# Performance work log

Measured on AMD Instinct MI355X. Metric: run time of the kernel, lower is better.

The kernel has to match this reference:

```python
import jax, jax.numpy as jnp
import numpy as np

NUM_EXPERTS = 8
TOP_K = 2
DIM = 1024
HIDDEN = 2048
TOKENS = 8192


def setup_inputs() -> dict:
    key = jax.random.key(0)
    k0, k1, k2, k3, k4 = jax.random.split(key, 5)
    x = jax.random.normal(k0, (TOKENS, DIM), dtype=jnp.float32)
    gate_w = jax.random.normal(k1, (NUM_EXPERTS, DIM), dtype=jnp.float32) * 0.02
    # SwiGLU expert weights, stacked over experts
    w1 = jax.random.normal(k2, (NUM_EXPERTS, DIM, HIDDEN), dtype=jnp.float32) * 0.02
    w3 = jax.random.normal(k3, (NUM_EXPERTS, DIM, HIDDEN), dtype=jnp.float32) * 0.02
    w2 = jax.random.normal(k4, (NUM_EXPERTS, HIDDEN, DIM), dtype=jnp.float32) * 0.02
    return {"x": x, "gate_w": gate_w, "w1": w1, "w3": w3, "w2": w2}


def reference(x, gate_w, w1, w3, w2):
    # x: [T, D]; gate_w: [E, D]; w1,w3: [E, D, H]; w2: [E, H, D]
    E = gate_w.shape[0]
    gate_logits = x @ gate_w.T                               # [T, E]
    topk_vals, topk_idx = jax.lax.top_k(gate_logits, TOP_K)  # [T, K]
    topk_w = jax.nn.softmax(topk_vals.astype(jnp.float32), axis=-1).astype(x.dtype)
    # per-token per-expert combine weight: sum_k w[t,k] * [sel[t,k]==e]  -> [T, E]
    combine = jnp.einsum('tk,tke->te', topk_w,
                         jax.nn.one_hot(topk_idx, E, dtype=x.dtype))
    # SwiGLU experts, computed per expert over all tokens then masked-combined
    h = jnp.einsum('td,edh->eth', x, w1)                     # [E, T, H]
    g = jnp.einsum('td,edh->eth', x, w3)                     # [E, T, H]
    y = jnp.einsum('eth,ehd->etd', jax.nn.silu(h) * g, w2)   # [E, T, D]
    return jnp.einsum('te,etd->td', combine, y)              # [T, D]
```

## Files before the change

### kernel.cpp

```cpp
#include <hip/hip_runtime.h>
#include <cstdint>
#include <cstddef>

#define T_TOKENS 8192
#define DIM      1024
#define HID      2048
#define NE       8
#define HCAP     17408

typedef __attribute__((ext_vector_type(8))) short short8;
typedef __attribute__((ext_vector_type(4))) short short4v;
typedef __attribute__((ext_vector_type(4))) float f32x4;

__device__ __forceinline__ unsigned short f2bf(float f) {
  unsigned int u = __builtin_bit_cast(unsigned int, f);
  u += 0x7fffu + ((u >> 16) & 1u);
  return (unsigned short)(u >> 16);
}

__device__ __forceinline__ void gload16(const void* g, void* lds) {
  __builtin_amdgcn_global_load_lds((const __attribute__((address_space(1))) void*)g,
                                   (__attribute__((address_space(3))) void*)lds,
                                   16, 0, 0);
}

#define PREP_GATE0 12288
__device__ __forceinline__ void transcvt_body(
    const float* __restrict__ in, unsigned short* __restrict__ out,
    int K, int N, int bx, int by, int e, float (*tile)[65], int tid) {
  int r  = tid >> 2;
  int c0 = (tid & 3) * 16;
  const float* src = in + ((size_t)e * K + by * 64 + r) * N + bx * 64 + c0;
#pragma unroll
  for (int j = 0; j < 4; j++) {
    float4 v = *(const float4*)(src + j * 4);
    tile[r][c0 + j * 4 + 0] = v.x; tile[r][c0 + j * 4 + 1] = v.y;
    tile[r][c0 + j * 4 + 2] = v.z; tile[r][c0 + j * 4 + 3] = v.w;
  }
  __syncthreads();
  short8 o0, o1;
#pragma unroll
  for (int j = 0; j < 8; j++) o0[j] = (short)f2bf(tile[c0 + j][r]);
#pragma unroll
  for (int j = 0; j < 8; j++) o1[j] = (short)f2bf(tile[c0 + 8 + j][r]);
  unsigned short* dst = out + ((size_t)e * N + bx * 64 + r) * K + by * 64 + c0;
  *(short8*)dst = o0;
  *(short8*)(dst + 8) = o1;
}

__global__ __launch_bounds__(256) void prep_kernel(
    const float* __restrict__ x, const float* __restrict__ gw,
    const float* __restrict__ w1, const float* __restrict__ w3,
    const float* __restrict__ w2,
    unsigned short* __restrict__ W1T, unsigned short* __restrict__ W3T,
    unsigned short* __restrict__ W2T,
    int2* __restrict__ sel, float2* __restrict__ wts,
    unsigned short* __restrict__ xb) {
  __shared__ float tile[64][65];
  int bid = blockIdx.x, tid = threadIdx.x;

  if (bid < PREP_GATE0) {
    if (bid < 4096) {
      int t = bid;
      transcvt_body(w1, W1T, DIM, HID, t % 32, (t / 32) % 16, t / 512, tile, tid);
    } else if (bid < 8192) {
      int t = bid - 4096;
      transcvt_body(w3, W3T, DIM, HID, t % 32, (t / 32) % 16, t / 512, tile, tid);
    } else {
      int t = bid - 8192;
      transcvt_body(w2, W2T, HID, DIM, t % 16, (t / 16) % 32, t / 512, tile, tid);
    }
    return;
  }

  int wid = tid >> 6, lane = tid & 63;
  int t = (bid - PREP_GATE0) * 4 + wid;
  const float* xr = x + (size_t)t * DIM;
  unsigned short* xo = xb + (size_t)t * DIM;
  double acc[NE];
#pragma unroll
  for (int e = 0; e < NE; e++) acc[e] = 0.0;
#pragma unroll
  for (int p = 0; p < 4; p++) {
    int idx = p * 256 + lane * 4;
    float4 xv = *(const float4*)(xr + idx);
    short4v o;
    o[0] = (short)f2bf(xv.x); o[1] = (short)f2bf(xv.y);
    o[2] = (short)f2bf(xv.z); o[3] = (short)f2bf(xv.w);
    *(short4v*)(xo + idx) = o;
#pragma unroll
    for (int e = 0; e < NE; e++) {
      float4 g = *(const float4*)(gw + e * DIM + idx);
      acc[e] += (double)xv.x * (double)g.x + (double)xv.y * (double)g.y
              + (double)xv.z * (double)g.z + (double)xv.w * (double)g.w;
    }
  }
#pragma unroll
  for (int e = 0; e < NE; e++) {
    double v = acc[e];
#pragma unroll
    for (int off = 32; off > 0; off >>= 1) v += __shfl_xor(v, off);
    acc[e] = v;
  }
  if (lane == 0) {
    float l[NE];
#pragma unroll
    for (int e = 0; e < NE; e++) l[e] = (float)acc[e];
    int i0 = 0; float v0 = l[0];
#pragma unroll
    for (int e = 1; e < NE; e++) if (l[e] > v0) { v0 = l[e]; i0 = e; }
    int i1 = -1; float v1 = -3.4e38f;
#pragma unroll
    for (int e = 0; e < NE; e++) if (e != i0 && l[e] > v1) { v1 = l[e]; i1 = e; }
    float ew = __expf(v1 - v0);
    float w0 = 1.0f / (1.0f + ew);
    float w1v = ew / (1.0f + ew);
    sel[t] = make_int2(i0, i1);
    wts[t] = make_float2(w0, w1v);
  }
}

__global__ void scatter_kernel(const int2* __restrict__ sel, const float2* __restrict__ wts,
                               int* __restrict__ cnt, int* __restrict__ btok,
                               float* __restrict__ bw) {
  __shared__ int hist[NE];
  __shared__ int base[NE];
  int tid = threadIdx.x;
  if (tid < NE) hist[tid] = 0;
  __syncthreads();
  int t = blockIdx.x * 256 + tid;
  int2 s = sel[t]; float2 w = wts[t];
  int p0 = atomicAdd(&hist[s.x], 1);
  int p1 = atomicAdd(&hist[s.y], 1);
  __syncthreads();
  if (tid < NE) base[tid] = atomicAdd(&cnt[tid], hist[tid]);
  __syncthreads();
  int o0 = base[s.x] + p0;
  btok[s.x * T_TOKENS + o0] = t; bw[s.x * T_TOKENS + o0] = w.x;
  int o1 = base[s.y] + p1;
  btok[s.y * T_TOKENS + o1] = t; bw[s.y * T_TOKENS + o1] = w.y;
}

__global__ __launch_bounds__(256, 2) void gemm1_kernel(
    const unsigned short* __restrict__ xb, const unsigned short* __restrict__ w1t,
    const unsigned short* __restrict__ w3t, const int* __restrict__ cnt,
    const int* __restrict__ btok, const unsigned short* __restrict__ zbuf,
    unsigned short* __restrict__ h) {
  int e = blockIdx.z;
  int cn = cnt[e];
  int pc = (cn + 127) & ~127;
  int mt = blockIdx.y;
  if (mt * 128 >= pc) return;
  int hoff = 0;
#pragma unroll
  for (int i = 0; i < NE; i++) { int pi = (cnt[i] + 127) & ~127; if (i < e) hoff += pi; }
  int nt = blockIdx.x;

  __shared__ short8 At8[1024];
  __shared__ short8 B18[512];
  __shared__ short8 B38[512];

  int tid = threadIdx.x, wid = tid >> 6, lane = tid & 63;
  int m0 = mt * 128;

  int swzcol = ((lane & 7) ^ (lane >> 3)) * 8;

  const unsigned short* asrc[4];
#pragma unroll
  for (int rd = 0; rd < 4; rd++) {
    int row = (rd * 4 + wid) * 8 + (lane >> 3);
    int r = m0 + row;
    asrc[rd] = (r < cn) ? (xb + (size_t)btok[e * T_TOKENS + r] * DIM + swzcol)
                        : (zbuf + swzcol);
  }
  const unsigned short* b1s[2]; const unsigned short* b3s[2];
#pragma unroll
  for (int rd = 0; rd < 2; rd++) {
    int row = (rd * 4 + wid) * 8 + (lane >> 3);
    size_t o = ((size_t)e * HID + nt * 64 + row) * DIM + swzcol;
    b1s[rd] = w1t + o; b3s[rd] = w3t + o;
  }

  f32x4 zero = {0.f, 0.f, 0.f, 0.f};
  f32x4 acc1[4][2], acc3[4][2];
#pragma unroll
  for (int m = 0; m < 4; m++)
#pragma unroll
    for (int n = 0; n < 2; n++) { acc1[m][n] = zero; acc3[m][n] = zero; }

  int wr = wid >> 1, wc = wid & 1;
  const char* At = (const char*)At8;
  const char* B1 = (const char*)B18;
  const char* B3 = (const char*)B38;
  int lxor = (lane & 7) << 4;

  for (int kt = 0; kt < DIM / 64; kt++) {
    int ko = kt * 64;
#pragma unroll
    for (int rd = 0; rd < 4; rd++)
      gload16(asrc[rd] + ko, (char*)At8 + (rd * 4 + wid) * 1024);
#pragma unroll
    for (int rd = 0; rd < 2; rd++) {
      gload16(b1s[rd] + ko, (char*)B18 + (rd * 4 + wid) * 1024);
      gload16(b3s[rd] + ko, (char*)B38 + (rd * 4 + wid) * 1024);
    }
    __syncthreads();
#pragma unroll
    for (int ks = 0; ks < 2; ks++) {
      int cb = (ks * 64 + (lane >> 4) * 16) ^ lxor;
      short8 a[4], f1[2], f3[2];
#pragma unroll
      for (int m = 0; m < 4; m++)
        a[m] = *(const short8*)(At + (wr * 64 + m * 16 + (lane & 15)) * 128 + cb);
#pragma unroll
      for (int n = 0; n < 2; n++) {
        int rb = (wc * 32 + n * 16 + (lane & 15)) * 128 + cb;
        f1[n] = *(const short8*)(B1 + rb);
        f3[n] = *(const short8*)(B3 + rb);
      }
#pragma unroll
      for (int m = 0; m < 4; m++)
#pragma unroll
        for (int n = 0; n < 2; n++) {
          acc1[m][n] = __builtin_amdgcn_mfma_f32_16x16x32_bf16(a[m], f1[n], acc1[m][n], 0, 0, 0);
          acc3[m][n] = __builtin_amdgcn_mfma_f32_16x16x32_bf16(a[m], f3[n], acc3[m][n], 0, 0, 0);
        }
    }
    __syncthreads();
  }

#pragma unroll
  for (int m = 0; m < 4; m++)
#pragma unroll
    for (int n = 0; n < 2; n++) {
#pragma unroll
      for (int j = 0; j < 4; j++) {
        float s1 = acc1[m][n][j], s3 = acc3[m][n][j];
        float hv = s1 / (1.0f + __expf(-s1)) * s3;
        int row = wr * 64 + m * 16 + (lane >> 4) * 4 + j;
        int col = nt * 64 + wc * 32 + n * 16 + (lane & 15);
        h[(size_t)(hoff + m0 + row) * HID + col] = f2bf(hv);
      }
    }
}

__global__ __launch_bounds__(256, 2) void gemm2_kernel(
    const unsigned short* __restrict__ h, const unsigned short* __restrict__ w2t,
    const int* __restrict__ cnt, const int* __restrict__ btok,
    const float* __restrict__ bw, float* __restrict__ out) {
  int e = blockIdx.z;
  int cn = cnt[e];
  int pc = (cn + 127) & ~127;
  int mt = blockIdx.y;
  if (mt * 128 >= pc) return;
  int hoff = 0;
#pragma unroll
  for (int i = 0; i < NE; i++) { int pi = (cnt[i] + 127) & ~127; if (i < e) hoff += pi; }
  int nt = blockIdx.x;

  __shared__ short8 At8[1024];
  __shared__ short8 Bt8[1024];

  int tid = threadIdx.x, wid = tid >> 6, lane = tid & 63;
  int m0 = mt * 128;

  int swzcol = ((lane & 7) ^ (lane >> 3)) * 8;

  const unsigned short* as[4]; const unsigned short* bs[4];
#pragma unroll
  for (int rd = 0; rd < 4; rd++) {
    int row = (rd * 4 + wid) * 8 + (lane >> 3);
    as[rd] = h + (size_t)(hoff + m0 + row) * HID + swzcol;
    bs[rd] = w2t + ((size_t)e * DIM + nt * 128 + row) * HID + swzcol;
  }

  f32x4 zero = {0.f, 0.f, 0.f, 0.f};
  f32x4 acc[4][4];
#pragma unroll
  for (int m = 0; m < 4; m++)
#pragma unroll
    for (int n = 0; n < 4; n++) acc[m][n] = zero;

  int wr = wid >> 1, wc = wid & 1;
  const char* At = (const char*)At8;
  const char* Bt = (const char*)Bt8;
  int lxor = (lane & 7) << 4;

  for (int kt = 0; kt < HID / 64; kt++) {
    int ko = kt * 64;
#pragma unroll
    for (int rd = 0; rd < 4; rd++) {
      gload16(as[rd] + ko, (char*)At8 + (rd * 4 + wid) * 1024);
      gload16(bs[rd] + ko, (char*)Bt8 + (rd * 4 + wid) * 1024);
    }
    __syncthreads();
#pragma unroll
    for (int ks = 0; ks < 2; ks++) {
      int cb = (ks * 64 + (lane >> 4) * 16) ^ lxor;
      short8 a[4], b[4];
#pragma unroll
      for (int m = 0; m < 4; m++)
        a[m] = *(const short8*)(At + (wr * 64 + m * 16 + (lane & 15)) * 128 + cb);
#pragma unroll
      for (int n = 0; n < 4; n++)
        b[n] = *(const short8*)(Bt + (wc * 64 + n * 16 + (lane & 15)) * 128 + cb);
#pragma unroll
      for (int m = 0; m < 4; m++)
#pragma unroll
        for (int n = 0; n < 4; n++)
          acc[m][n] = __builtin_amdgcn_mfma_f32_16x16x32_bf16(a[m], b[n], acc[m][n], 0, 0, 0);
    }
    __syncthreads();
  }

#pragma unroll
  for (int m = 0; m < 4; m++)
#pragma unroll
    for (int j = 0; j < 4; j++) {
      int r = m0 + wr * 64 + m * 16 + (lane >> 4) * 4 + j;
      if (r < cn) {
        int t = btok[e * T_TOKENS + r];
        float w = bw[e * T_TOKENS + r];
        size_t ob = (size_t)t * DIM + nt * 128 + wc * 64 + (lane & 15);
#pragma unroll
        for (int n = 0; n < 4; n++)
          atomicAdd(out + ob + n * 16, w * acc[m][n][j]);
      }
    }
}

extern "C" void kernel_launch(void* const* d_in, const int* in_sizes, int n_in,
                              void* d_out, int out_size, void* d_ws, size_t ws_size,
                              hipStream_t stream) {
  const float* x  = (const float*)d_in[0];
  const float* gw = (const float*)d_in[1];
  const float* w1 = (const float*)d_in[2];
  const float* w3 = (const float*)d_in[3];
  const float* w2 = (const float*)d_in[4];
  float* out = (float*)d_out;

  char* ws = (char*)d_ws;
  unsigned short* W1T = (unsigned short*)ws;
  unsigned short* W3T = W1T + (size_t)NE * HID * DIM;
  unsigned short* W2T = W3T + (size_t)NE * HID * DIM;
  unsigned short* XB  = W2T + (size_t)NE * DIM * HID;
  unsigned short* H   = XB + (size_t)T_TOKENS * DIM;
  int*   TOK = (int*)(H + (size_t)HCAP * HID);
  float* BW  = (float*)(TOK + NE * T_TOKENS);
  int*   CNT = (int*)(BW + NE * T_TOKENS);
  unsigned short* ZBUF = (unsigned short*)(CNT + 16);
  int2*   SEL = (int2*)(ZBUF + 1024);
  float2* WTS = (float2*)(SEL + T_TOKENS);

  hipMemsetAsync(d_out, 0, (size_t)out_size * sizeof(float), stream);
  hipMemsetAsync(CNT, 0, 16 * sizeof(int) + 1024 * sizeof(unsigned short), stream);

  prep_kernel<<<14336, 256, 0, stream>>>(x, gw, w1, w3, w2, W1T, W3T, W2T, SEL, WTS, XB);
  scatter_kernel<<<T_TOKENS / 256, 256, 0, stream>>>(SEL, WTS, CNT, TOK, BW);
  gemm1_kernel<<<dim3(HID / 64, 64, NE), 256, 0, stream>>>(XB, W1T, W3T, CNT, TOK, ZBUF, H);
  gemm2_kernel<<<dim3(DIM / 128, 64, NE), 256, 0, stream>>>(H, W2T, CNT, TOK, BW, out);
}
```

Before: 357.4 us.

## Replace gemm2 atomic scatter with bf16 staging buffer and gather combine kernel

```diff
diff --git a/kernel.cpp b/kernel.cpp
--- a/kernel.cpp
+++ b/kernel.cpp
@@ -16,6 +16,11 @@
   unsigned int u = __builtin_bit_cast(unsigned int, f);
   u += 0x7fffu + ((u >> 16) & 1u);
   return (unsigned short)(u >> 16);
+}
+
+__device__ __forceinline__ float bf2f(unsigned short b) {
+  unsigned int u = ((unsigned int)b) << 16;
+  return __builtin_bit_cast(float, u);
 }
 
 __device__ __forceinline__ void gload16(const void* g, void* lds) {
@@ -55,7 +60,8 @@
     unsigned short* __restrict__ W1T, unsigned short* __restrict__ W3T,
     unsigned short* __restrict__ W2T,
     int2* __restrict__ sel, float2* __restrict__ wts,
-    unsigned short* __restrict__ xb) {
+    unsigned short* __restrict__ xb,
+    int* __restrict__ cnt, unsigned short* __restrict__ zbuf) {
   __shared__ float tile[64][65];
   int bid = blockIdx.x, tid = threadIdx.x;
 
@@ -73,6 +79,12 @@
     return;
   }
 
+  if (bid == PREP_GATE0) {
+    if (tid < 16) cnt[tid] = 0;
+    short8 z = {0, 0, 0, 0, 0, 0, 0, 0};
+    if (tid * 8 < 1024) *(short8*)(zbuf + tid * 8) = z;
+  }
+
   int wid = tid >> 6, lane = tid & 63;
   int t = (bid - PREP_GATE0) * 4 + wid;
   const float* xr = x + (size_t)t * DIM;
@@ -122,7 +134,7 @@
 
 __global__ void scatter_kernel(const int2* __restrict__ sel, const float2* __restrict__ wts,
                                int* __restrict__ cnt, int* __restrict__ btok,
-                               float* __restrict__ bw) {
+                               float* __restrict__ bw, int2* __restrict__ pos) {
   __shared__ int hist[NE];
   __shared__ int base[NE];
   int tid = threadIdx.x;
@@ -139,6 +151,7 @@
   btok[s.x * T_TOKENS + o0] = t; bw[s.x * T_TOKENS + o0] = w.x;
   int o1 = base[s.y] + p1;
   btok[s.y * T_TOKENS + o1] = t; bw[s.y * T_TOKENS + o1] = w.y;
+  pos[t] = make_int2(o0, o1);
 }
 
 __global__ __launch_bounds__(256, 2) void gemm1_kernel(
@@ -246,8 +259,8 @@
 
 __global__ __launch_bounds__(256, 2) void gemm2_kernel(
     const unsigned short* __restrict__ h, const unsigned short* __restrict__ w2t,
-    const int* __restrict__ cnt, const int* __restrict__ btok,
-    const float* __restrict__ bw, float* __restrict__ out) {
+    const int* __restrict__ cnt, const float* __restrict__ bw,
+    unsigned short* __restrict__ Y) {
   int e = blockIdx.z;
   int cn = cnt[e];
   int pc = (cn + 127) & ~127;
@@ -319,14 +332,41 @@
     for (int j = 0; j < 4; j++) {
       int r = m0 + wr * 64 + m * 16 + (lane >> 4) * 4 + j;
       if (r < cn) {
-        int t = btok[e * T_TOKENS + r];
         float w = bw[e * T_TOKENS + r];
-        size_t ob = (size_t)t * DIM + nt * 128 + wc * 64 + (lane & 15);
+        size_t yb = (size_t)(hoff + r) * DIM + nt * 128 + wc * 64 + (lane & 15);
 #pragma unroll
         for (int n = 0; n < 4; n++)
-          atomicAdd(out + ob + n * 16, w * acc[m][n][j]);
+          Y[yb + n * 16] = f2bf(w * acc[m][n][j]);
       }
     }
+}
+
+__global__ __launch_bounds__(256) void combine_kernel(
+    const unsigned short* __restrict__ Y, const int2* __restrict__ sel,
+    const int2* __restrict__ pos, const int* __restrict__ cnt,
+    float* __restrict__ out) {
+  int hoffs[NE + 1];
+  hoffs[0] = 0;
+#pragma unroll
+  for (int i = 0; i < NE; i++) hoffs[i + 1] = hoffs[i] + ((cnt[i] + 127) & ~127);
+
+  int tid = threadIdx.x;
+  int t = blockIdx.x * 2 + (tid >> 7);
+  int d0 = (tid & 127) * 8;
+  int2 s = sel[t];
+  int2 p = pos[t];
+  size_t g0 = (size_t)(hoffs[s.x] + p.x) * DIM + d0;
+  size_t g1 = (size_t)(hoffs[s.y] + p.y) * DIM + d0;
+  short8 a = *(const short8*)(Y + g0);
+  short8 b = *(const short8*)(Y + g1);
+  float* o = out + (size_t)t * DIM + d0;
+  f32x4 lo, hi;
+#pragma unroll
+  for (int j = 0; j < 4; j++) lo[j] = bf2f((unsigned short)a[j]) + bf2f((unsigned short)b[j]);
+#pragma unroll
+  for (int j = 0; j < 4; j++) hi[j] = bf2f((unsigned short)a[4 + j]) + bf2f((unsigned short)b[4 + j]);
+  *(f32x4*)o = lo;
+  *(f32x4*)(o + 4) = hi;
 }
 
 extern "C" void kernel_launch(void* const* d_in, const int* in_sizes, int n_in,
@@ -351,12 +391,13 @@
   unsigned short* ZBUF = (unsigned short*)(CNT + 16);
   int2*   SEL = (int2*)(ZBUF + 1024);
   float2* WTS = (float2*)(SEL + T_TOKENS);
-
-  hipMemsetAsync(d_out, 0, (size_t)out_size * sizeof(float), stream);
-  hipMemsetAsync(CNT, 0, 16 * sizeof(int) + 1024 * sizeof(unsigned short), stream);
-
-  prep_kernel<<<14336, 256, 0, stream>>>(x, gw, w1, w3, w2, W1T, W3T, W2T, SEL, WTS, XB);
-  scatter_kernel<<<T_TOKENS / 256, 256, 0, stream>>>(SEL, WTS, CNT, TOK, BW);
+  int2*   POS = (int2*)(WTS + T_TOKENS);
+  unsigned short* Y = W1T;
+
+  prep_kernel<<<14336, 256, 0, stream>>>(x, gw, w1, w3, w2, W1T, W3T, W2T,
+                                         SEL, WTS, XB, CNT, ZBUF);
+  scatter_kernel<<<T_TOKENS / 256, 256, 0, stream>>>(SEL, WTS, CNT, TOK, BW, POS);
   gemm1_kernel<<<dim3(HID / 64, 64, NE), 256, 0, stream>>>(XB, W1T, W3T, CNT, TOK, ZBUF, H);
-  gemm2_kernel<<<dim3(DIM / 128, 64, NE), 256, 0, stream>>>(H, W2T, CNT, TOK, BW, out);
-}
+  gemm2_kernel<<<dim3(DIM / 128, 64, NE), 256, 0, stream>>>(H, W2T, CNT, BW, Y);
+  combine_kernel<<<T_TOKENS / 2, 256, 0, stream>>>(Y, SEL, POS, CNT, out);
+}
```

New measurement: 337.3 us. 1.06x faster.
